# Performance work log

Hardware: AMD Instinct MI355X
Metric: run time of the kernel (lower is better)

Reference implementation:

```python
import jax, jax.numpy as jnp
import numpy as np

N_USERS = 200000
N_ITEMS = 100000
DIM = 64
N_EDGES = 2000000
N_LAYERS = 3


def setup_inputs() -> dict:
    key = jax.random.key(0)
    k1, k2, k3, k4 = jax.random.split(key, 4)
    return {
        "user_emb": jax.random.normal(k1, (N_USERS, DIM), dtype=jnp.float32) * 0.01,
        "item_emb": jax.random.normal(k2, (N_ITEMS, DIM), dtype=jnp.float32) * 0.01,
        "edge_rows": jax.random.randint(k3, (N_EDGES,), 0, N_USERS, dtype=jnp.int32),
        "edge_cols": jax.random.randint(k4, (N_EDGES,), 0, N_ITEMS, dtype=jnp.int32),
        "n_layers": N_LAYERS,
    }


def reference(user_emb, item_emb, edge_rows, edge_cols, n_layers):
    nu = user_emb.shape[0]
    ni = item_emb.shape[0]
    n_nodes = nu + ni

    # _normalize_adj_m: symmetric deg^-0.5 normalization of bipartite graph
    ones = jnp.ones(edge_rows.shape, dtype=jnp.float32)
    deg_u = 1e-7 + jax.ops.segment_sum(ones, edge_rows, num_segments=nu)
    deg_i = 1e-7 + jax.ops.segment_sum(ones, edge_cols, num_segments=ni)
    vals = (deg_u ** -0.5)[edge_rows] * (deg_i ** -0.5)[edge_cols]

    # Symmetric adjacency over n_nodes: (u, i+nu) edges plus flipped copies
    cols_off = edge_cols + nu
    dst = jnp.concatenate([edge_rows, cols_off])  # [2E]
    src = jnp.concatenate([cols_off, edge_rows])  # [2E]
    all_vals = jnp.concatenate([vals, vals])       # [2E]

    ego = jnp.concatenate([user_emb, item_emb], axis=0)  # [n_nodes, d]
    eps = 1e-8
    ego_norm = jnp.maximum(jnp.linalg.norm(ego, axis=-1), eps)

    x = ego
    acc = jnp.zeros_like(ego)
    for _ in range(n_layers):
        # SpMM: A @ x via gather + segment_sum over edges
        msg = all_vals[:, None] * x[src]                       # [2E, d]
        x = jax.ops.segment_sum(msg, dst, num_segments=n_nodes)  # [n_nodes, d]
        # cosine-similarity reweighting against ego embeddings
        w = jnp.sum(x * ego, axis=-1) / (
            jnp.maximum(jnp.linalg.norm(x, axis=-1), eps) * ego_norm)
        x = w[:, None] * x
        acc = acc + x

    return acc[:nu], acc[nu:]
```

## Files before the change

kernel.cpp:

```cpp
#include <hip/hip_runtime.h>

#define DIM 64

#define SPAN 256
#define NSHIFT 8
#define MAXNB 2048
#define BCAP 8192
#define EPT 16
#define EPB (256 * EPT)

typedef __attribute__((ext_vector_type(4))) _Float16 half4;
typedef __attribute__((ext_vector_type(8))) _Float16 half8;

__global__ void bucket_scatter2(const int* __restrict__ rows, const int* __restrict__ cols,
                                int* __restrict__ bucket_cnt, int* __restrict__ rec,
                                int nu, int nb, int E) {
    __shared__ int hist[MAXNB];
    __shared__ int base[MAXNB];
    int t = threadIdx.x;
    for (int b = t; b < MAXNB; b += 256) hist[b] = 0;
    __syncthreads();
    int e0 = blockIdx.x * EPB;
    int e1 = min(e0 + EPB, E);
    for (int e = e0 + t; e < e1; e += 256) {
        int r = rows[e];
        int c = nu + cols[e];
        atomicAdd(&hist[r >> NSHIFT], 1);
        atomicAdd(&hist[c >> NSHIFT], 1);
    }
    __syncthreads();
    for (int b = t; b < nb; b += 256) {
        int h = hist[b];
        int off = 0;
        if (h) off = atomicAdd(&bucket_cnt[b * 16], h);
        if (off > BCAP) off = BCAP;
        base[b] = b * BCAP + off;
        hist[b] = 0;
    }
    __syncthreads();
    for (int e = e0 + t; e < e1; e += 256) {
        int r = rows[e];
        int c = nu + cols[e];
        int b1 = r >> NSHIFT;
        int p1 = atomicAdd(&hist[b1], 1);
        rec[base[b1] + p1] = (r & (SPAN - 1)) | (c << NSHIFT);
        int b2 = c >> NSHIFT;
        int p2 = atomicAdd(&hist[b2], 1);
        rec[base[b2] + p2] = (c & (SPAN - 1)) | (r << NSHIFT);
    }
}

__global__ void bucket_fill3(const int* __restrict__ bucket_cnt, const int* __restrict__ rec,
                             int* __restrict__ colidx, int* __restrict__ row_ptr,
                             const float4* __restrict__ ue, const float4* __restrict__ ie,
                             half4* __restrict__ x0, int nu, int nn, int nb) {
    __shared__ int cnt[SPAN];
    __shared__ int lds[256];
    int t = threadIdx.x;
    int b = blockIdx.x;
    int gbase;
    {
        int part = 0;
        for (int i = t; i < b; i += 256) part += bucket_cnt[i * 16];
        lds[t] = part; __syncthreads();
        for (int off = 128; off >= 1; off >>= 1) {
            if (t < off) lds[t] += lds[t + off];
            __syncthreads();
        }
        gbase = lds[0];
        __syncthreads();
    }
    int nrec = bucket_cnt[b * 16];
    const int* r0 = rec + (size_t)b * BCAP;

    cnt[t] = 0;
    __syncthreads();
    for (int i = t; i < nrec; i += 256)
        atomicAdd(&cnt[r0[i] & (SPAN - 1)], 1);
    __syncthreads();
    int d = cnt[t];
    lds[t] = d; __syncthreads();
    for (int off = 1; off < 256; off <<= 1) {
        int add = (t >= off) ? lds[t - off] : 0;
        __syncthreads();
        lds[t] += add;
        __syncthreads();
    }
    int excl = lds[t] - d;
    int node = (b << NSHIFT) + t;
    if (node < nn) row_ptr[node] = gbase + excl;
    if (b == nb - 1 && t == 0) row_ptr[nn] = gbase + nrec;
    cnt[t] = excl;
    lds[t] = 0;
    __syncthreads();
    for (int i = t; i < nrec; i += 256) {
        int v = r0[i];
        int dl = v & (SPAN - 1);
        int pos = gbase + cnt[dl] + atomicAdd(&lds[dl], 1);
        colidx[pos] = v >> NSHIFT;
    }
    __syncthreads();
    for (int i = t; i < SPAN * 16; i += 256) {
        int nl = i >> 4;
        int node2 = (b << NSHIFT) + nl;
        if (node2 >= nn) break;
        int li = i & 15;
        float dn = rsqrtf(1e-7f + (float)lds[nl]);
        size_t o = (size_t)node2 * 16 + li;
        float4 v = (node2 < nu) ? ue[o] : ie[o - (size_t)nu * 16];
        half4 h;
        h.x = (_Float16)(v.x * dn); h.y = (_Float16)(v.y * dn);
        h.z = (_Float16)(v.z * dn); h.w = (_Float16)(v.w * dn);
        x0[o] = h;
    }
}

template<bool EGO16>
__global__ void spmm_fused(const int* __restrict__ row_ptr, const int* __restrict__ colidx,
                           const half8* __restrict__ xp, const half8* __restrict__ x0,
                           const float4* __restrict__ eu, const float4* __restrict__ ei,
                           half8* __restrict__ xn, float4* __restrict__ acc,
                           int nu, int nn, int first, int last) {
    int gid  = (int)(blockIdx.x * blockDim.x + threadIdx.x) >> 3;
    int li   = threadIdx.x & 7;
    bool valid = gid < nn;
    int node = valid ? gid : nn - 1;
    int start = row_ptr[node];
    int deg   = row_ptr[node + 1] - start;

    const half8 hz = {(_Float16)0, (_Float16)0, (_Float16)0, (_Float16)0,
                      (_Float16)0, (_Float16)0, (_Float16)0, (_Float16)0};
    half8 a0 = hz, a1 = hz, a2 = hz, a3 = hz;
    const unsigned li16 = (unsigned)li << 4;
    const char* xpb = (const char*)xp;
    int j = 0;
    for (; j + 4 <= deg; j += 4) {
        int s0 = colidx[start + j];
        int s1 = colidx[start + j + 1];
        int s2 = colidx[start + j + 2];
        int s3 = colidx[start + j + 3];
        a0 += *(const half8*)(xpb + (((unsigned)s0 << 7) + li16));
        a1 += *(const half8*)(xpb + (((unsigned)s1 << 7) + li16));
        a2 += *(const half8*)(xpb + (((unsigned)s2 << 7) + li16));
        a3 += *(const half8*)(xpb + (((unsigned)s3 << 7) + li16));
    }
    if (j < deg) {
        int laste = start + deg - 1;
        int s0 = colidx[start + j];
        int s1 = colidx[min(start + j + 1, laste)];
        int s2 = colidx[min(start + j + 2, laste)];
        a0 += *(const half8*)(xpb + (((unsigned)s0 << 7) + li16));
        if (j + 1 < deg) a1 += *(const half8*)(xpb + (((unsigned)s1 << 7) + li16));
        if (j + 2 < deg) a2 += *(const half8*)(xpb + (((unsigned)s2 << 7) + li16));
    }
    a0 += a1; a2 += a3; a0 += a2;

    float dn = rsqrtf(1e-7f + (float)deg);
    float xv[8];
#pragma unroll
    for (int k = 0; k < 8; k++) xv[k] = (float)a0[k] * dn;

    float ev[8];
    if constexpr (EGO16) {
        half8 e = *(const half8*)((const char*)x0 + (((size_t)node << 7) + li16));
#pragma unroll
        for (int k = 0; k < 8; k++) ev[k] = (float)e[k];
    } else {
        size_t o32 = (size_t)node * 16 + 2 * li;
        float4 e0 = (node < nu) ? eu[o32] : ei[o32 - (size_t)nu * 16];
        float4 e1 = (node < nu) ? eu[o32 + 1] : ei[o32 + 1 - (size_t)nu * 16];
        ev[0] = e0.x; ev[1] = e0.y; ev[2] = e0.z; ev[3] = e0.w;
        ev[4] = e1.x; ev[5] = e1.y; ev[6] = e1.z; ev[7] = e1.w;
    }
    float dp = 0.f, np = 0.f, ep = 0.f;
#pragma unroll
    for (int k = 0; k < 8; k++) {
        dp += xv[k] * ev[k];
        np += xv[k] * xv[k];
        ep += ev[k] * ev[k];
    }
#pragma unroll
    for (int m = 1; m <= 4; m <<= 1) {
        dp += __shfl_xor(dp, m, 64);
        np += __shfl_xor(np, m, 64);
        ep += __shfl_xor(ep, m, 64);
    }
    float en = EGO16 ? fmaxf(sqrtf(ep), 1e-8f * dn) : fmaxf(sqrtf(ep), 1e-8f);
    float w = dp / (fmaxf(sqrtf(np), 1e-8f) * en);

    if (valid) {
        if (!last) {
            half8 h;
#pragma unroll
            for (int k = 0; k < 8; k++) h[k] = (_Float16)(w * xv[k] * dn);
            *(half8*)((char*)xn + (((size_t)node << 7) + li16)) = h;
        }
        size_t o = (size_t)node * 16 + 2 * li;
        float4 f0 = make_float4(w * xv[0], w * xv[1], w * xv[2], w * xv[3]);
        float4 f1 = make_float4(w * xv[4], w * xv[5], w * xv[6], w * xv[7]);
        if (first) {
            acc[o] = f0;
            acc[o + 1] = f1;
        } else {
            float4 t0 = acc[o], t1 = acc[o + 1];
            acc[o]     = make_float4(t0.x + f0.x, t0.y + f0.y, t0.z + f0.z, t0.w + f0.w);
            acc[o + 1] = make_float4(t1.x + f1.x, t1.y + f1.y, t1.z + f1.z, t1.w + f1.w);
        }
    }
}

extern "C" void kernel_launch(void* const* d_in, const int* in_sizes, int n_in,
                              void* d_out, int out_size, void* d_ws, size_t ws_size,
                              hipStream_t stream) {
    const float* uemb = (const float*)d_in[0];
    const float* iemb = (const float*)d_in[1];
    const int*   rows = (const int*)d_in[2];
    const int*   cols = (const int*)d_in[3];

    const int nu = in_sizes[0] / DIM;
    const int ni = in_sizes[1] / DIM;
    const int E  = in_sizes[2];
    const int nn = nu + ni;
    const int nb = (nn + SPAN - 1) >> NSHIFT;

    const size_t hbuf = (size_t)nn * 16 * sizeof(half4);
    const size_t rec_bytes = (size_t)nb * BCAP * sizeof(int);
    const size_t bufB = hbuf > rec_bytes ? hbuf : rec_bytes;
    const size_t cid_bytes = (size_t)2 * E * sizeof(int);
    const size_t rp_bytes  = (size_t)(nn + 1) * sizeof(int);
    const size_t bc_bytes  = (size_t)MAXNB * 16 * sizeof(int);
    const size_t need3 = hbuf + bufB + hbuf + cid_bytes + rp_bytes + bc_bytes + 1024;
    const bool ego16 = (ws_size >= need3);

    char* ws = (char*)d_ws;
    half4* A = (half4*)ws;
    half4* B = (half4*)(ws + hbuf);
    half4* C = nullptr;
    char* after;
    if (ego16) { C = (half4*)(ws + hbuf + bufB); after = ws + hbuf + bufB + hbuf; }
    else       { after = ws + hbuf + bufB; }
    int* colidx   = (int*)after;
    int* row_ptr  = (int*)(after + cid_bytes);
    int* bkt_cnt  = (int*)(after + cid_bytes + rp_bytes);
    int* rec      = (int*)B;

    hipMemsetAsync(bkt_cnt, 0, bc_bytes, stream);
    bucket_scatter2<<<(E + EPB - 1) / EPB, 256, 0, stream>>>(rows, cols, bkt_cnt, rec, nu, nb, E);
    bucket_fill3<<<nb, 256, 0, stream>>>(bkt_cnt, rec, colidx, row_ptr,
                                         (const float4*)uemb, (const float4*)iemb, A, nu, nn, nb);

    unsigned gs = (unsigned)(((size_t)nn * 8 + 255) / 256);
    float4* out = (float4*)d_out;
    if (ego16) {
        spmm_fused<true><<<gs, 256, 0, stream>>>(row_ptr, colidx, (const half8*)A, (const half8*)A,
                                                 nullptr, nullptr, (half8*)B, out, nu, nn, 1, 0);
        spmm_fused<true><<<gs, 256, 0, stream>>>(row_ptr, colidx, (const half8*)B, (const half8*)A,
                                                 nullptr, nullptr, (half8*)C, out, nu, nn, 0, 0);
        spmm_fused<true><<<gs, 256, 0, stream>>>(row_ptr, colidx, (const half8*)C, (const half8*)A,
                                                 nullptr, nullptr, nullptr, out, nu, nn, 0, 1);
    } else {
        spmm_fused<false><<<gs, 256, 0, stream>>>(row_ptr, colidx, (const half8*)A, nullptr,
                                                  (const float4*)uemb, (const float4*)iemb,
                                                  (half8*)B, out, nu, nn, 1, 0);
        spmm_fused<false><<<gs, 256, 0, stream>>>(row_ptr, colidx, (const half8*)B, nullptr,
                                                  (const float4*)uemb, (const float4*)iemb,
                                                  (half8*)A, out, nu, nn, 0, 0);
        spmm_fused<false><<<gs, 256, 0, stream>>>(row_ptr, colidx, (const half8*)A, nullptr,
                                                  (const float4*)uemb, (const float4*)iemb,
                                                  nullptr, out, nu, nn, 0, 1);
    }
}
```

Baseline: 529.4 us.

## Split bucket base scan and prescaling out of bucket_fill into separate kernels

Replaces the per-block redundant prefix sum over all previous bucket counts, which gets quadratic in total, with one single-block scan kernel that writes bucket bases and the final row_ptr entry. The degree-scaled fp16 conversion of the embeddings moves out of bucket_fill3 into its own elementwise kernel that reads degrees from row_ptr. Edges per block in the scatter kernel are doubled. This adds two kernel launches and an extra pass over row_ptr in exchange for removing redundant global reads and shrinking the fill kernel.

```diff
diff --git a/kernel.cpp b/kernel.cpp
--- a/kernel.cpp
+++ b/kernel.cpp
@@ -6,7 +6,7 @@
 #define NSHIFT 8
 #define MAXNB 2048
 #define BCAP 8192
-#define EPT 16
+#define EPT 32
 #define EPB (256 * EPT)
 
 typedef __attribute__((ext_vector_type(4))) _Float16 half4;
@@ -50,28 +50,38 @@
     }
 }
 
-__global__ void bucket_fill3(const int* __restrict__ bucket_cnt, const int* __restrict__ rec,
-                             int* __restrict__ colidx, int* __restrict__ row_ptr,
-                             const float4* __restrict__ ue, const float4* __restrict__ ie,
-                             half4* __restrict__ x0, int nu, int nn, int nb) {
+__global__ void bucket_scan(const int* __restrict__ bucket_cnt, int* __restrict__ bucket_base,
+                            int* __restrict__ row_ptr_end, int nb) {
+    __shared__ int lds[1024];
+    int t = threadIdx.x;
+    int i0 = 2 * t, i1 = 2 * t + 1;
+    int v0 = (i0 < nb) ? bucket_cnt[i0 * 16] : 0;
+    int v1 = (i1 < nb) ? bucket_cnt[i1 * 16] : 0;
+    int s = v0 + v1;
+    lds[t] = s; __syncthreads();
+    for (int off = 1; off < 1024; off <<= 1) {
+        int add = (t >= off) ? lds[t - off] : 0;
+        __syncthreads();
+        lds[t] += add;
+        __syncthreads();
+    }
+    int excl = lds[t] - s;
+    if (i0 < nb) bucket_base[i0] = excl;
+    if (i1 < nb) bucket_base[i1] = excl + v0;
+    if (i0 == nb - 1) *row_ptr_end = excl + v0;
+    if (i1 == nb - 1) *row_ptr_end = excl + v0 + v1;
+}
+
+__global__ void bucket_fill3(const int* __restrict__ bucket_cnt, const int* __restrict__ bucket_base,
+                             const int* __restrict__ rec, int* __restrict__ colidx,
+                             int* __restrict__ row_ptr, int nn) {
     __shared__ int cnt[SPAN];
     __shared__ int lds[256];
     int t = threadIdx.x;
     int b = blockIdx.x;
-    int gbase;
-    {
-        int part = 0;
-        for (int i = t; i < b; i += 256) part += bucket_cnt[i * 16];
-        lds[t] = part; __syncthreads();
-        for (int off = 128; off >= 1; off >>= 1) {
-            if (t < off) lds[t] += lds[t + off];
-            __syncthreads();
-        }
-        gbase = lds[0];
-        __syncthreads();
-    }
     int nrec = bucket_cnt[b * 16];
     const int* r0 = rec + (size_t)b * BCAP;
+    int gbase = bucket_base[b];
 
     cnt[t] = 0;
     __syncthreads();
@@ -89,7 +99,6 @@
     int excl = lds[t] - d;
     int node = (b << NSHIFT) + t;
     if (node < nn) row_ptr[node] = gbase + excl;
-    if (b == nb - 1 && t == 0) row_ptr[nn] = gbase + nrec;
     cnt[t] = excl;
     lds[t] = 0;
     __syncthreads();
@@ -99,20 +108,21 @@
         int pos = gbase + cnt[dl] + atomicAdd(&lds[dl], 1);
         colidx[pos] = v >> NSHIFT;
     }
-    __syncthreads();
-    for (int i = t; i < SPAN * 16; i += 256) {
-        int nl = i >> 4;
-        int node2 = (b << NSHIFT) + nl;
-        if (node2 >= nn) break;
-        int li = i & 15;
-        float dn = rsqrtf(1e-7f + (float)lds[nl]);
-        size_t o = (size_t)node2 * 16 + li;
-        float4 v = (node2 < nu) ? ue[o] : ie[o - (size_t)nu * 16];
-        half4 h;
-        h.x = (_Float16)(v.x * dn); h.y = (_Float16)(v.y * dn);
-        h.z = (_Float16)(v.z * dn); h.w = (_Float16)(v.w * dn);
-        x0[o] = h;
-    }
+}
+
+__global__ void prescale_kernel(const float4* __restrict__ ue, const float4* __restrict__ ie,
+                                const int* __restrict__ row_ptr, half4* __restrict__ xp,
+                                int nu, int nn) {
+    size_t i = (size_t)blockIdx.x * blockDim.x + threadIdx.x;
+    if (i >= (size_t)nn * 16) return;
+    int node = (int)(i >> 4);
+    float4 v = (node < nu) ? ue[i] : ie[i - (size_t)nu * 16];
+    int d = row_ptr[node + 1] - row_ptr[node];
+    float dn = rsqrtf(1e-7f + (float)d);
+    half4 h;
+    h.x = (_Float16)(v.x * dn); h.y = (_Float16)(v.y * dn);
+    h.z = (_Float16)(v.z * dn); h.w = (_Float16)(v.w * dn);
+    xp[i] = h;
 }
 
 template<bool EGO16>
@@ -229,7 +239,8 @@
     const size_t cid_bytes = (size_t)2 * E * sizeof(int);
     const size_t rp_bytes  = (size_t)(nn + 1) * sizeof(int);
     const size_t bc_bytes  = (size_t)MAXNB * 16 * sizeof(int);
-    const size_t need3 = hbuf + bufB + hbuf + cid_bytes + rp_bytes + bc_bytes + 1024;
+    const size_t bb_bytes  = (size_t)MAXNB * sizeof(int);
+    const size_t need3 = hbuf + bufB + hbuf + cid_bytes + rp_bytes + bc_bytes + bb_bytes + 1024;
     const bool ego16 = (ws_size >= need3);
 
     char* ws = (char*)d_ws;
@@ -242,12 +253,19 @@
     int* colidx   = (int*)after;
     int* row_ptr  = (int*)(after + cid_bytes);
     int* bkt_cnt  = (int*)(after + cid_bytes + rp_bytes);
+    int* bkt_base = (int*)(after + cid_bytes + rp_bytes + bc_bytes);
     int* rec      = (int*)B;
 
     hipMemsetAsync(bkt_cnt, 0, bc_bytes, stream);
     bucket_scatter2<<<(E + EPB - 1) / EPB, 256, 0, stream>>>(rows, cols, bkt_cnt, rec, nu, nb, E);
-    bucket_fill3<<<nb, 256, 0, stream>>>(bkt_cnt, rec, colidx, row_ptr,
-                                         (const float4*)uemb, (const float4*)iemb, A, nu, nn, nb);
+    bucket_scan<<<1, 1024, 0, stream>>>(bkt_cnt, bkt_base, row_ptr + nn, nb);
+    bucket_fill3<<<nb, 256, 0, stream>>>(bkt_cnt, bkt_base, rec, colidx, row_ptr, nn);
+
+    {
+        size_t thr = (size_t)nn * 16;
+        prescale_kernel<<<(unsigned)((thr + 255) / 256), 256, 0, stream>>>(
+            (const float4*)uemb, (const float4*)iemb, row_ptr, A, nu, nn);
+    }
 
     unsigned gs = (unsigned)(((size_t)nn * 8 + 255) / 256);
     float4* out = (float4*)d_out;
```

Result: faster. 507.5 us (-4.1%).
